# Optimization experiments

Measured on AMD Instinct MI355X. Metric: run time of the kernel, lower is better.

## Reference

```python
import jax, jax.numpy as jnp
import numpy as np

NUM_BITS = 8
PACKET = 1024
LENGTH = 8192
VDD = 1.0
VR = VDD / 2 ** NUM_BITS   # Vr = Vdd / 2**q_bits
VREF = VR
DELTA = 1e-30
W_SIZE = NUM_BITS * (NUM_BITS + 1) // 2  # 36


def setup_inputs() -> dict:
    key = jax.random.key(0)
    kx, kw = jax.random.split(key)
    x = jax.random.uniform(kx, (LENGTH, PACKET), dtype=jnp.float32)
    W = jax.random.normal(kw, (W_SIZE,), dtype=jnp.float32)
    return {"x": x, "W": W}


def reference(x, W):
    # Bit-serial SAR ADC recurrence. noisy_inference=False -> W_noisy = W.
    nb = NUM_BITS
    Qbits = [None] * nb          # each [length, packet]
    m = W.shape[0] - 1
    for j in reversed(range(nb)):
        bit_sum = W[m] * VREF    # scalar, broadcasts over [length, packet]
        m -= 1
        for k in range(j + 1, nb):
            bit_sum = bit_sum + (Qbits[k] + 1.0) * 0.5 * W[m] * VR
            m -= 1
        Qbits[j] = jnp.sign(x - bit_sum + DELTA)
    Q = jnp.stack(Qbits, axis=-1)                 # [length, packet, num_bits]
    # q = sum_b (Q_b + 1)/2 * Vr * 2^b
    scales = VR * (2.0 ** jnp.arange(nb, dtype=jnp.float32))  # [num_bits]
    q = jnp.einsum('lpb,b->lp', (Q + 1.0) * 0.5, scales)
    return (q.astype(jnp.float32), Q.astype(jnp.float32), W)
```

## Files before the change

### kernel.cpp

```cpp
#include <hip/hip_runtime.h>


typedef float f4 __attribute__((ext_vector_type(4)));

constexpr int NB     = 8;
constexpr int TOTAL  = 8192 * 1024;
constexpr int Q_OFF  = TOTAL;
constexpr int W_OFF  = TOTAL * (NB + 1);
constexpr float VRC  = 1.0f / 256.0f;
constexpr int NBLOCKS = TOTAL / 1024;

__global__ __launch_bounds__(256) void sar_adc_kernel(
    const float* __restrict__ x,
    const float* __restrict__ W,
    float* __restrict__ out)
{
    __shared__ f4 lds[2048];

    float w[36];
#pragma unroll
    for (int i = 0; i < 36; ++i) w[i] = W[i];

    if (blockIdx.x == 0 && threadIdx.x < 36) {
        out[W_OFF + threadIdx.x] = w[threadIdx.x];
    }

    const f4* __restrict__ x4 = (const f4*)x;
    f4* __restrict__ q4 = (f4*)out;
    f4* __restrict__ Q4 = (f4*)(out + Q_OFF);

    const int t    = threadIdx.x;
    const int tile = blockIdx.x;
    const int vin  = tile * 256 + t;

    const f4 xv = __builtin_nontemporal_load(&x4[vin]);
    const float xe[4] = {xv.x, xv.y, xv.z, xv.w};
    float qout[4];
    float Qb[4][NB];

#pragma unroll
    for (int e = 0; e < 4; ++e) {
        const float xs = xe[e] * 256.0f;
        bool bit[NB];
        int m = 35;
#pragma unroll
        for (int j = NB - 1; j >= 0; --j) {
            float bs = w[m]; m--;
#pragma unroll
            for (int k = j + 1; k < NB; ++k) {
                bs += bit[k] ? w[m] : 0.0f;
                m--;
            }
            bit[j] = (xs - bs) >= 0.0f;
        }
        int n = 0;
#pragma unroll
        for (int b = 0; b < NB; ++b) {
            Qb[e][b] = bit[b] ? 1.0f : -1.0f;
            n += bit[b] ? (1 << b) : 0;
        }
        qout[e] = (float)n * VRC;
    }

    {
        f4 qv = {qout[0], qout[1], qout[2], qout[3]};
        __builtin_nontemporal_store(qv, &q4[vin]);
    }

#pragma unroll
    for (int i = 0; i < 8; ++i) {
        const int e  = i >> 1;
        const int b0 = (i & 1) * 4;
        f4 qb = {Qb[e][b0 + 0], Qb[e][b0 + 1], Qb[e][b0 + 2], Qb[e][b0 + 3]};
        lds[t * 8 + (i ^ (t & 7))] = qb;
    }

    __syncthreads();

    const int qbase = tile * 2048;
#pragma unroll
    for (int s = 0; s < 8; ++s) {
        const int f   = s * 256 + t;
        const int tw  = f >> 3;
        const int iw  = f & 7;
        __builtin_nontemporal_store(lds[tw * 8 + (iw ^ (tw & 7))], &Q4[qbase + f]);
    }
}

extern "C" void kernel_launch(void* const* d_in, const int* in_sizes, int n_in,
                              void* d_out, int out_size, void* d_ws, size_t ws_size,
                              hipStream_t stream) {
    const float* x = (const float*)d_in[0];
    const float* W = (const float*)d_in[1];
    float* out = (float*)d_out;

    sar_adc_kernel<<<NBLOCKS, 256, 0, stream>>>(x, W, out);
}
```

Baseline: 155.8 us.

## Split SAR ADC into code-compute kernel and bit-expansion kernel via workspace

Splits the fused kernel in two. The first kernel computes the 8-bit codes and q and writes packed byte codes to the workspace. The second kernel reads those bytes and expands each bit into ±1 floats for Q with coalesced stores, so the LDS transpose and the barrier go away. The fused path is kept as a fallback when the workspace is too small. The price is an extra kernel launch plus an 8 MB workspace write and re-read.

```diff
diff --git a/kernel.cpp b/kernel.cpp
--- a/kernel.cpp
+++ b/kernel.cpp
@@ -1,22 +1,23 @@
 #include <hip/hip_runtime.h>
+#include <stdint.h>
 
 
 typedef float f4 __attribute__((ext_vector_type(4)));
 
 constexpr int NB     = 8;
 constexpr int TOTAL  = 8192 * 1024;
+constexpr int NVEC   = TOTAL / 4;
 constexpr int Q_OFF  = TOTAL;
 constexpr int W_OFF  = TOTAL * (NB + 1);
 constexpr float VRC  = 1.0f / 256.0f;
-constexpr int NBLOCKS = TOTAL / 1024;
+constexpr int NBLOCKS = NVEC / 256;
 
-__global__ __launch_bounds__(256) void sar_adc_kernel(
+__global__ __launch_bounds__(256) void quant_code_kernel(
     const float* __restrict__ x,
     const float* __restrict__ W,
-    float* __restrict__ out)
+    float* __restrict__ out,
+    uint32_t* __restrict__ codes4)
 {
-    __shared__ f4 lds[2048];
-
     float w[36];
 #pragma unroll
     for (int i = 0; i < 36; ++i) w[i] = W[i];
@@ -27,16 +28,13 @@
 
     const f4* __restrict__ x4 = (const f4*)x;
     f4* __restrict__ q4 = (f4*)out;
-    f4* __restrict__ Q4 = (f4*)(out + Q_OFF);
 
-    const int t    = threadIdx.x;
-    const int tile = blockIdx.x;
-    const int vin  = tile * 256 + t;
+    const int v = blockIdx.x * 256 + threadIdx.x;
 
-    const f4 xv = __builtin_nontemporal_load(&x4[vin]);
+    const f4 xv = __builtin_nontemporal_load(&x4[v]);
     const float xe[4] = {xv.x, xv.y, xv.z, xv.w};
     float qout[4];
-    float Qb[4][NB];
+    uint32_t code = 0;
 
 #pragma unroll
     for (int e = 0; e < 4; ++e) {
@@ -55,34 +53,89 @@
         }
         int n = 0;
 #pragma unroll
-        for (int b = 0; b < NB; ++b) {
-            Qb[e][b] = bit[b] ? 1.0f : -1.0f;
-            n += bit[b] ? (1 << b) : 0;
-        }
+        for (int b = 0; b < NB; ++b) n += bit[b] ? (1 << b) : 0;
         qout[e] = (float)n * VRC;
+        code |= (uint32_t)n << (8 * e);
     }
 
     {
         f4 qv = {qout[0], qout[1], qout[2], qout[3]};
-        __builtin_nontemporal_store(qv, &q4[vin]);
+        __builtin_nontemporal_store(qv, &q4[v]);
     }
+    __builtin_nontemporal_store(code, &codes4[v]);
+}
+
+__global__ __launch_bounds__(256) void expand_kernel(
+    const uint8_t* __restrict__ codes,
+    float* __restrict__ out)
+{
+    f4* __restrict__ Q4 = (f4*)(out + Q_OFF);
+    const int tile = blockIdx.x;
+    const int t    = threadIdx.x;
+    const int ebase = tile * 1024;
+    const size_t qbase = (size_t)tile * 2048;
 
 #pragma unroll
+    for (int s = 0; s < 8; ++s) {
+        const int f = s * 256 + t;
+        const uint32_t c = codes[ebase + (f >> 1)];
+        const int b0 = (f & 1) * 4;
+        f4 qb = { (c >> (b0 + 0)) & 1 ? 1.0f : -1.0f,
+                  (c >> (b0 + 1)) & 1 ? 1.0f : -1.0f,
+                  (c >> (b0 + 2)) & 1 ? 1.0f : -1.0f,
+                  (c >> (b0 + 3)) & 1 ? 1.0f : -1.0f };
+        __builtin_nontemporal_store(qb, &Q4[qbase + f]);
+    }
+}
+
+__global__ __launch_bounds__(256) void sar_adc_fused(
+    const float* __restrict__ x,
+    const float* __restrict__ W,
+    float* __restrict__ out)
+{
+    __shared__ f4 lds[2048];
+    float w[36];
+#pragma unroll
+    for (int i = 0; i < 36; ++i) w[i] = W[i];
+    if (blockIdx.x == 0 && threadIdx.x < 36) out[W_OFF + threadIdx.x] = w[threadIdx.x];
+
+    const f4* __restrict__ x4 = (const f4*)x;
+    f4* __restrict__ q4 = (f4*)out;
+    f4* __restrict__ Q4 = (f4*)(out + Q_OFF);
+    const int t = threadIdx.x, tile = blockIdx.x;
+    const int vin = tile * 256 + t;
+
+    const f4 xv = __builtin_nontemporal_load(&x4[vin]);
+    const float xe[4] = {xv.x, xv.y, xv.z, xv.w};
+    float qout[4]; float Qb[4][NB];
+#pragma unroll
+    for (int e = 0; e < 4; ++e) {
+        const float xs = xe[e] * 256.0f;
+        bool bit[NB]; int m = 35;
+#pragma unroll
+        for (int j = NB - 1; j >= 0; --j) {
+            float bs = w[m]; m--;
+#pragma unroll
+            for (int k = j + 1; k < NB; ++k) { bs += bit[k] ? w[m] : 0.0f; m--; }
+            bit[j] = (xs - bs) >= 0.0f;
+        }
+        int n = 0;
+#pragma unroll
+        for (int b = 0; b < NB; ++b) { Qb[e][b] = bit[b] ? 1.0f : -1.0f; n += bit[b] ? (1 << b) : 0; }
+        qout[e] = (float)n * VRC;
+    }
+    { f4 qv = {qout[0], qout[1], qout[2], qout[3]}; __builtin_nontemporal_store(qv, &q4[vin]); }
+#pragma unroll
     for (int i = 0; i < 8; ++i) {
-        const int e  = i >> 1;
-        const int b0 = (i & 1) * 4;
-        f4 qb = {Qb[e][b0 + 0], Qb[e][b0 + 1], Qb[e][b0 + 2], Qb[e][b0 + 3]};
+        const int e = i >> 1, b0 = (i & 1) * 4;
+        f4 qb = {Qb[e][b0+0], Qb[e][b0+1], Qb[e][b0+2], Qb[e][b0+3]};
         lds[t * 8 + (i ^ (t & 7))] = qb;
     }
-
     __syncthreads();
-
     const int qbase = tile * 2048;
 #pragma unroll
     for (int s = 0; s < 8; ++s) {
-        const int f   = s * 256 + t;
-        const int tw  = f >> 3;
-        const int iw  = f & 7;
+        const int f = s * 256 + t, tw = f >> 3, iw = f & 7;
         __builtin_nontemporal_store(lds[tw * 8 + (iw ^ (tw & 7))], &Q4[qbase + f]);
     }
 }
@@ -94,5 +147,11 @@
     const float* W = (const float*)d_in[1];
     float* out = (float*)d_out;
 
-    sar_adc_kernel<<<NBLOCKS, 256, 0, stream>>>(x, W, out);
+    if (ws_size >= (size_t)TOTAL) {
+        uint32_t* codes4 = (uint32_t*)d_ws;
+        quant_code_kernel<<<NBLOCKS, 256, 0, stream>>>(x, W, out, codes4);
+        expand_kernel<<<NBLOCKS, 256, 0, stream>>>((const uint8_t*)d_ws, out);
+    } else {
+        sar_adc_fused<<<NBLOCKS, 256, 0, stream>>>(x, W, out);
+    }
 }
```

Result: slower. 167.1 us (+7.3%).
